# Optimization experiments

Measured on AMD Instinct MI355X. Metric: run time of the kernel, lower is better.

## Reference

```python
import jax, jax.numpy as jnp
import numpy as np

BATCH, L, IN_DIM, HID, STATE, MLP, OUT, NUM_LAYERS = 16, 2048, 64, 256, 256, 1024, 128, 4
MAX_PHASE = 2.0 * np.pi


def setup_inputs() -> dict:
    key = jax.random.key(0)
    ks = iter(jax.random.split(key, 32))
    x = jax.random.normal(next(ks), (BATCH, L, IN_DIM), dtype=jnp.float32)
    # embedding Linear(IN_DIM -> HID)
    emb_W = jax.random.normal(next(ks), (HID, IN_DIM), dtype=jnp.float32) / np.sqrt(IN_DIM)
    emb_b = jnp.zeros((HID,), dtype=jnp.float32)
    # LRU params per layer (r_min=0, r_max=1, max_phase=2pi)
    u1 = jax.random.uniform(next(ks), (NUM_LAYERS, STATE), minval=1e-4, maxval=1.0)
    u2 = jax.random.uniform(next(ks), (NUM_LAYERS, STATE), minval=1e-4, maxval=1.0)
    nu_log = jnp.log(-0.5 * jnp.log(u1))
    theta_log = jnp.log(MAX_PHASE * u2)
    lam_abs = jnp.exp(-jnp.exp(nu_log))
    gamma_log = jnp.log(jnp.sqrt(1.0 - lam_abs ** 2))
    B_re = jax.random.normal(next(ks), (NUM_LAYERS, STATE, HID)) / np.sqrt(2 * HID)
    B_im = jax.random.normal(next(ks), (NUM_LAYERS, STATE, HID)) / np.sqrt(2 * HID)
    C_re = jax.random.normal(next(ks), (NUM_LAYERS, HID, STATE)) / np.sqrt(STATE)
    C_im = jax.random.normal(next(ks), (NUM_LAYERS, HID, STATE)) / np.sqrt(STATE)
    D = jax.random.normal(next(ks), (NUM_LAYERS, HID))
    # block MLP: Linear(STATE->MLP), GELU, Linear(MLP->HID)
    Wh = jax.random.normal(next(ks), (NUM_LAYERS, MLP, STATE)) / np.sqrt(STATE)
    bh = jnp.zeros((NUM_LAYERS, MLP), dtype=jnp.float32)
    Wo = jax.random.normal(next(ks), (NUM_LAYERS, HID, MLP)) / np.sqrt(MLP)
    bo = jnp.zeros((NUM_LAYERS, HID), dtype=jnp.float32)
    # output Linear(HID -> OUT)
    out_W = jax.random.normal(next(ks), (OUT, HID), dtype=jnp.float32) / np.sqrt(HID)
    out_b = jnp.zeros((OUT,), dtype=jnp.float32)
    return {"x": x, "emb_W": emb_W, "emb_b": emb_b, "nu_log": nu_log,
            "theta_log": theta_log, "gamma_log": gamma_log, "B_re": B_re,
            "B_im": B_im, "C_re": C_re, "C_im": C_im, "D": D,
            "Wh": Wh, "bh": bh, "Wo": Wo, "bo": bo,
            "out_W": out_W, "out_b": out_b}


def _binop(ei, ej):
    a_i, bu_i = ei
    a_j, bu_j = ej
    return a_j * a_i, a_j * bu_i + bu_j


def _lru(x, nu, th, gl, Bre, Bim, Cre, Cim, D):
    # x: (B, L, H) real; state diag recurrence in complex64
    lam = jnp.exp(-jnp.exp(nu) + 1j * jnp.exp(th))               # (S,)
    B_norm = (Bre + 1j * Bim) * jnp.exp(gl)[:, None]             # (S, H)
    Bu = jnp.einsum("blh,sh->bls", x.astype(B_norm.dtype), B_norm)  # (B, L, S)
    Lam = jnp.broadcast_to(lam, Bu.shape)
    _, states = jax.lax.associative_scan(_binop, (Lam, Bu), axis=1)
    C = Cre + 1j * Cim                                           # (H, S)
    y = jnp.einsum("bls,hs->blh", states, C).real + D * x        # (B, L, H)
    return y


def reference(x, emb_W, emb_b, nu_log, theta_log, gamma_log, B_re, B_im,
              C_re, C_im, D, Wh, bh, Wo, bo, out_W, out_b):
    h = x @ emb_W.T + emb_b                                      # (B, L, HID)
    for l in range(NUM_LAYERS):
        y = _lru(h, nu_log[l], theta_log[l], gamma_log[l],
                 B_re[l], B_im[l], C_re[l], C_im[l], D[l])
        z = jax.nn.gelu(y @ Wh[l].T + bh[l], approximate=False)  # exact GELU as torch
        h = z @ Wo[l].T + bo[l] + y                              # residual
    return h @ out_W.T + out_b                                   # (B, L, OUT)
```

## Files before the change

kernel.cpp:

```cpp
#include <hip/hip_runtime.h>
#include <hip/hip_bf16.h>
#include <math.h>

typedef __hip_bfloat16 bf16;
typedef __attribute__((ext_vector_type(8))) short bf16x8;
typedef __attribute__((ext_vector_type(4))) float f32x4;

#define BATCH   16
#define SEQLEN  2048
#define INDIM   64
#define HIDD    256
#define STATE_D 256
#define MLPD    1024
#define OUTD    128
#define NLAYERS 4
#define M_TOK   (BATCH*SEQLEN)
#define CHUNK   64
#define NCHUNK  (SEQLEN/CHUNK)

__device__ float g_carry[512*512];
__device__ bf16  g_hb [(size_t)M_TOK*256];
__device__ bf16  g_yb [(size_t)M_TOK*256];
__device__ bf16  g_bub[(size_t)M_TOK*512];
__device__ bf16  g_zb [(size_t)M_TOK*1024];
__device__ bf16  g_Bnb[NLAYERS*512*256];
__device__ bf16  g_Cwb[NLAYERS*256*512];
__device__ bf16  g_Whb[NLAYERS*1024*256];
__device__ bf16  g_Wob[NLAYERS*256*1024];

#define SB_HB  0
#define SB_YB  1
#define SB_BUB 2
#define SB_ZB  3
#define SB_BNB 4
#define SB_CWB 5
#define SB_WHB 6
#define SB_WOB 7

__device__ __forceinline__ bf16* bufb(int sel){
  switch(sel){
    case SB_HB:  return g_hb;  case SB_YB:  return g_yb;
    case SB_BUB: return g_bub; case SB_ZB:  return g_zb;
    case SB_BNB: return g_Bnb; case SB_CWB: return g_Cwb;
    case SB_WHB: return g_Whb; default:     return g_Wob; }
}

__device__ __forceinline__ void gld_lds16(const void* g, void* l){
  __builtin_amdgcn_global_load_lds(
      (const __attribute__((address_space(1))) unsigned int*)g,
      (__attribute__((address_space(3))) unsigned int*)l, 16, 0, 0);
}

__device__ __forceinline__ float fast_gelu(float v){
  const float x  = v * 0.70710678118654752f;
  const float ax = fabsf(x);
  const float t  = __builtin_amdgcn_rcpf(fmaf(0.3275911f, ax, 1.0f));
  float p = fmaf(t, 1.061405429f, -1.453152027f);
  p = fmaf(t, p, 1.421413741f);
  p = fmaf(t, p, -0.284496736f);
  p = fmaf(t, p, 0.254829592f);
  p = p * t;
  const float e = __expf(-ax * ax);
  const float erf_ax = fmaf(-p, e, 1.0f);
  const float erf_x  = copysignf(erf_ax, x);
  return 0.5f * v * (1.0f + erf_x);
}

#define RPSTR 136

template<int ACT, int FLAGS>
__global__ __launch_bounds__(256, 6) void mfma_gemm(
    int aSel, int lda, int wSel, int wOff, int ldw,
    int oSel, int ldc,
    const float* __restrict__ bias,
    int rSel, int ldres,
    const float* __restrict__ dscale,
    int K)
{
  const bf16* A = bufb(aSel);
  const bf16* W = bufb(wSel) + wOff;
  bf16* OB = bufb(oSel);
  const bf16* res = (rSel >= 0) ? bufb(rSel) : nullptr;

  __shared__ __align__(16) unsigned short lds[12288];
  unsigned short* As = lds;
  unsigned short* Ws = lds + 4096;

  const int gx = gridDim.x;
  const int nwg = gx * gridDim.y;
  const int orig = blockIdx.y * gx + blockIdx.x;
  const int q = nwg >> 3, r = nwg & 7;
  const int xcd = orig & 7, idx = orig >> 3;
  const int wg = (xcd < r ? xcd*(q+1) : r*(q+1) + (xcd-r)*q) + idx;
  const int bx = wg % gx, by = wg / gx;

  const int tid  = threadIdx.x;
  const int row0 = by * 64, col0 = bx * 128;
  const int lane = tid & 63;
  const int m16  = lane & 15, quad = lane >> 4;
  const int wv   = tid >> 6;
  const int wm   = (wv & 1) * 32, wn = (wv >> 1) * 64;

  const int rlo = wv*16 + (lane >> 2);
  const int sg  = ((lane & 3) ^ ((rlo >> 1) & 3)) * 8;
  const bf16* ga = &A[(size_t)(row0 + rlo)*lda + sg];
  const bf16* gw = &W[(size_t)(col0 + rlo)*ldw + sg];
  const size_t w64 = (size_t)64 * ldw;

  auto STAGE = [&](int bb, int k0){
    unsigned short* Ab = As + bb*2048;
    unsigned short* Wb = Ws + bb*4096;
    gld_lds16(ga + k0,       Ab + wv*512);
    gld_lds16(gw + k0,       Wb + wv*512);
    gld_lds16(gw + k0 + w64, Wb + 2048 + wv*512);
  };

  f32x4 acc[2][4] = {};
  const int nt = K >> 5;

  STAGE(0, 0); STAGE(1, 32);

  for (int t = 0; t < nt; ++t){
    const int b = t & 1;
    if (t + 1 < nt) asm volatile("s_waitcnt vmcnt(3)" ::: "memory");
    else            asm volatile("s_waitcnt vmcnt(0)" ::: "memory");
    __builtin_amdgcn_s_barrier();

    const unsigned short* Ab = As + b*2048;
    const unsigned short* Wb = Ws + b*4096;
    bf16x8 af[2], wf[4];
    #pragma unroll
    for (int i = 0; i < 2; i++){
      const int rA = wm + 16*i + m16;
      af[i] = *reinterpret_cast<const bf16x8*>(&Ab[rA*32 + ((quad ^ ((rA>>1)&3))<<3)]);
    }
    #pragma unroll
    for (int j = 0; j < 4; j++){
      const int rW = wn + 16*j + m16;
      wf[j] = *reinterpret_cast<const bf16x8*>(&Wb[rW*32 + ((quad ^ ((rW>>1)&3))<<3)]);
    }
    asm volatile("s_waitcnt lgkmcnt(0)" ::: "memory");
    __builtin_amdgcn_sched_barrier(0);
    __builtin_amdgcn_s_barrier();

    if (t + 2 < nt) STAGE(b, (t + 2) << 5);

    __builtin_amdgcn_s_setprio(1);
    #pragma unroll
    for (int i = 0; i < 2; i++)
      #pragma unroll
      for (int j = 0; j < 4; j++)
        acc[i][j] = __builtin_amdgcn_mfma_f32_16x16x32_bf16(af[i], wf[j], acc[i][j], 0, 0, 0);
    __builtin_amdgcn_s_setprio(0);
  }

  #pragma unroll
  for (int i = 0; i < 2; i++){
    #pragma unroll
    for (int j = 0; j < 4; j++){
      const int lcol = wn + 16*j + m16;
      const int col  = col0 + lcol;
      #pragma unroll
      for (int r2 = 0; r2 < 4; r2++){
        const int lrow = wm + 16*i + quad*4 + r2;
        const int row  = row0 + lrow;
        float v = acc[i][j][r2];
        if (FLAGS & 1) v += bias[col];
        if (ACT == 1)  v = fast_gelu(v);
        if (FLAGS & 2) v += __bfloat162float(res[(size_t)row*ldres + col]);
        if (FLAGS & 4) v += dscale[col] * __bfloat162float(res[(size_t)row*ldres + col]);
        bf16 bv = __float2bfloat16(v);
        lds[lrow*RPSTR + lcol] = *reinterpret_cast<unsigned short*>(&bv);
      }
    }
  }
  __syncthreads();

  {
    const int rr  = tid >> 4;
    const int c16 = (tid & 15) * 8;
    #pragma unroll
    for (int s = 0; s < 4; s++){
      const int orow = s*16 + rr;
      uint4 d = *reinterpret_cast<const uint4*>(&lds[orow*RPSTR + c16]);
      *reinterpret_cast<uint4*>(OB + (size_t)(row0 + orow)*ldc + col0 + c16) = d;
    }
  }
}

__global__ __launch_bounds__(256) void emb_gemm(
    const float* __restrict__ x, const float* __restrict__ W,
    const float* __restrict__ b)
{
  __shared__ __align__(16) float Asx[16][68];
  __shared__ __align__(16) float Wsx[16][68];
  const int tid = threadIdx.x;
  const int tx = tid & 15, ty = tid >> 4;
  const int row0 = blockIdx.y * 64, col0 = blockIdx.x * 64;
  const int lc = tid & 15, lr = tid >> 4;
  float acc[4][4] = {};
  for (int k0 = 0; k0 < INDIM; k0 += 16){
    #pragma unroll
    for (int i = 0; i < 4; i++){
      Asx[lc][lr + 16*i] = x[(size_t)(row0 + lr + 16*i)*INDIM + k0 + lc];
      Wsx[lc][lr + 16*i] = W[(size_t)(col0 + lr + 16*i)*INDIM + k0 + lc];
    }
    __syncthreads();
    #pragma unroll
    for (int k = 0; k < 16; k++){
      float4 av = *reinterpret_cast<const float4*>(&Asx[k][ty*4]);
      float4 bv = *reinterpret_cast<const float4*>(&Wsx[k][tx*4]);
      float a[4] = {av.x, av.y, av.z, av.w};
      float b2[4] = {bv.x, bv.y, bv.z, bv.w};
      #pragma unroll
      for (int i = 0; i < 4; i++)
        #pragma unroll
        for (int j = 0; j < 4; j++)
          acc[i][j] = fmaf(a[i], b2[j], acc[i][j]);
    }
    __syncthreads();
  }
  #pragma unroll
  for (int i = 0; i < 4; i++){
    const int r = row0 + ty*4 + i;
    #pragma unroll
    for (int j = 0; j < 4; j++){
      const int cn = col0 + tx*4 + j;
      g_hb[(size_t)r*HIDD + cn] = __float2bfloat16(acc[i][j] + b[cn]);
    }
  }
}

__global__ __launch_bounds__(256) void out_gemm(
    const float* __restrict__ W, const float* __restrict__ b,
    float* __restrict__ out)
{
  __shared__ __align__(16) float Asx[16][68];
  __shared__ __align__(16) float Wsx[16][68];
  const int tid = threadIdx.x;
  const int tx = tid & 15, ty = tid >> 4;
  const int row0 = blockIdx.y * 64, col0 = blockIdx.x * 64;
  const int lc = tid & 15, lr = tid >> 4;
  float acc[4][4] = {};
  for (int k0 = 0; k0 < HIDD; k0 += 16){
    #pragma unroll
    for (int i = 0; i < 4; i++){
      Asx[lc][lr + 16*i] = __bfloat162float(g_hb[(size_t)(row0 + lr + 16*i)*HIDD + k0 + lc]);
      Wsx[lc][lr + 16*i] = W[(size_t)(col0 + lr + 16*i)*HIDD + k0 + lc];
    }
    __syncthreads();
    #pragma unroll
    for (int k = 0; k < 16; k++){
      float4 av = *reinterpret_cast<const float4*>(&Asx[k][ty*4]);
      float4 bv = *reinterpret_cast<const float4*>(&Wsx[k][tx*4]);
      float a[4] = {av.x, av.y, av.z, av.w};
      float b2[4] = {bv.x, bv.y, bv.z, bv.w};
      #pragma unroll
      for (int i = 0; i < 4; i++)
        #pragma unroll
        for (int j = 0; j < 4; j++)
          acc[i][j] = fmaf(a[i], b2[j], acc[i][j]);
    }
    __syncthreads();
  }
  #pragma unroll
  for (int i = 0; i < 4; i++){
    const int r = row0 + ty*4 + i;
    #pragma unroll
    for (int j = 0; j < 4; j++){
      const int cn = col0 + tx*4 + j;
      out[(size_t)r*OUTD + cn] = acc[i][j] + b[cn];
    }
  }
}

__device__ __forceinline__ void lam_of(const float* __restrict__ nu_log,
                                       const float* __restrict__ th_log,
                                       int s, float& lr, float& li)
{
  float nu  = expf(nu_log[s]);
  float th  = expf(th_log[s]);
  float mag = expf(-nu);
  lr = mag * cosf(th);
  li = mag * sinf(th);
}

__global__ __launch_bounds__(256) void scan_local(
    const float* __restrict__ nu_log, const float* __restrict__ th_log)
{
  const int blk = blockIdx.x;
  const int s   = threadIdx.x;
  float lr, li; lam_of(nu_log, th_log, s, lr, li);
  float ar = 0.f, ai = 0.f;
  size_t base = (size_t)blk * CHUNK * 512 + s;
  for (int t = 0; t < CHUNK; t++){
    float br = __bfloat162float(g_bub[base + (size_t)t*512]);
    float bi = __bfloat162float(g_bub[base + (size_t)t*512 + 256]);
    float nr = fmaf(lr, ar, fmaf(-li, ai, br));
    float ni = fmaf(lr, ai, fmaf( li, ar, bi));
    ar = nr; ai = ni;
  }
  g_carry[(size_t)blk*512 + s]       = ar;
  g_carry[(size_t)blk*512 + 256 + s] = ai;
}

__global__ __launch_bounds__(256) void scan_fix(
    const float* __restrict__ nu_log, const float* __restrict__ th_log)
{
  const int blk = blockIdx.x;
  const int c   = blk & (NCHUNK - 1);
  const int s   = threadIdx.x;
  float lr, li; lam_of(nu_log, th_log, s, lr, li);
  float cr = 0.f, ci = 0.f;
  if (c > 0){
    float Tr = lr, Ti = li;
    #pragma unroll
    for (int i = 0; i < 6; i++){ float nr = Tr*Tr - Ti*Ti; Ti = 2.f*Tr*Ti; Tr = nr; }
    const int bstart = blk - c;
    for (int j = 0; j < c; j++){
      float er = g_carry[(size_t)(bstart + j)*512 + s];
      float ei = g_carry[(size_t)(bstart + j)*512 + 256 + s];
      float nr = fmaf(Tr, cr, fmaf(-Ti, ci, er));
      float ni = fmaf(Tr, ci, fmaf( Ti, cr, ei));
      cr = nr; ci = ni;
    }
  }
  float ar = cr, ai = ci;
  size_t base = (size_t)blk * CHUNK * 512 + s;
  for (int t = 0; t < CHUNK; t++){
    size_t o = base + (size_t)t*512;
    float br = __bfloat162float(g_bub[o]);
    float bi = __bfloat162float(g_bub[o + 256]);
    float nr = fmaf(lr, ar, fmaf(-li, ai, br));
    float ni = fmaf(lr, ai, fmaf( li, ar, bi));
    ar = nr; ai = ni;
    g_bub[o]       = __float2bfloat16(ar);
    g_bub[o + 256] = __float2bfloat16(ai);
  }
}

__global__ __launch_bounds__(256) void pack_B(
    const float* __restrict__ Bre, const float* __restrict__ Bim,
    const float* __restrict__ gl)
{
  int idx = blockIdx.x * 256 + threadIdx.x;
  int l = idx >> 16, within = idx & 65535;
  int s = within >> 8;
  float g = expf(gl[l*STATE_D + s]);
  g_Bnb[(size_t)l*131072 + within]         = __float2bfloat16(Bre[idx] * g);
  g_Bnb[(size_t)l*131072 + 65536 + within] = __float2bfloat16(Bim[idx] * g);
}

__global__ __launch_bounds__(256) void pack_C(
    const float* __restrict__ Cre, const float* __restrict__ Cim)
{
  int idx = blockIdx.x * 256 + threadIdx.x;
  int l = idx >> 16, within = idx & 65535;
  int h = within >> 8, s = within & 255;
  g_Cwb[(size_t)l*131072 + (size_t)h*512 + s]       = __float2bfloat16( Cre[idx]);
  g_Cwb[(size_t)l*131072 + (size_t)h*512 + 256 + s] = __float2bfloat16(-Cim[idx]);
}

__global__ __launch_bounds__(256) void conv_bf16(
    const float* __restrict__ src, int dstSel, int n)
{
  int i = blockIdx.x * 256 + threadIdx.x;
  if (i < n) bufb(dstSel)[i] = __float2bfloat16(src[i]);
}

extern "C" void kernel_launch(void* const* d_in, const int* in_sizes, int n_in,
                              void* d_out, int out_size, void* d_ws, size_t ws_size,
                              hipStream_t stream)
{
  (void)d_ws; (void)ws_size; (void)out_size; (void)n_in; (void)in_sizes;
  const float* x      = (const float*)d_in[0];
  const float* emb_W  = (const float*)d_in[1];
  const float* emb_b  = (const float*)d_in[2];
  const float* nu_log = (const float*)d_in[3];
  const float* th_log = (const float*)d_in[4];
  const float* ga_log = (const float*)d_in[5];
  const float* B_re   = (const float*)d_in[6];
  const float* B_im   = (const float*)d_in[7];
  const float* C_re   = (const float*)d_in[8];
  const float* C_im   = (const float*)d_in[9];
  const float* Dv     = (const float*)d_in[10];
  const float* Wh     = (const float*)d_in[11];
  const float* bh     = (const float*)d_in[12];
  const float* Wo     = (const float*)d_in[13];
  const float* bo     = (const float*)d_in[14];
  const float* out_W  = (const float*)d_in[15];
  const float* out_b  = (const float*)d_in[16];

  const dim3 blk(256);

  pack_B<<<dim3(NLAYERS*256), blk, 0, stream>>>(B_re, B_im, ga_log);
  pack_C<<<dim3(NLAYERS*256), blk, 0, stream>>>(C_re, C_im);
  conv_bf16<<<dim3(NLAYERS*1024), blk, 0, stream>>>(Wh, SB_WHB, NLAYERS*262144);
  conv_bf16<<<dim3(NLAYERS*1024), blk, 0, stream>>>(Wo, SB_WOB, NLAYERS*262144);

  emb_gemm<<<dim3(HIDD/64, M_TOK/64), blk, 0, stream>>>(x, emb_W, emb_b);

  for (int l = 0; l < NLAYERS; l++){
    mfma_gemm<0, 0><<<dim3(4, M_TOK/64), blk, 0, stream>>>(
        SB_HB, HIDD, SB_BNB, l*131072, HIDD, SB_BUB, 512,
        nullptr, -1, 0, nullptr, HIDD);

    scan_local<<<dim3(M_TOK/CHUNK), blk, 0, stream>>>(nu_log + l*STATE_D, th_log + l*STATE_D);
    scan_fix  <<<dim3(M_TOK/CHUNK), blk, 0, stream>>>(nu_log + l*STATE_D, th_log + l*STATE_D);

    mfma_gemm<0, 4><<<dim3(2, M_TOK/64), blk, 0, stream>>>(
        SB_BUB, 512, SB_CWB, l*131072, 512, SB_YB, HIDD,
        nullptr, SB_HB, HIDD, Dv + l*HIDD, 512);

    mfma_gemm<1, 1><<<dim3(8, M_TOK/64), blk, 0, stream>>>(
        SB_YB, HIDD, SB_WHB, l*262144, STATE_D, SB_ZB, MLPD,
        bh + l*MLPD, -1, 0, nullptr, STATE_D);

    mfma_gemm<0, 3><<<dim3(2, M_TOK/64), blk, 0, stream>>>(
        SB_ZB, MLPD, SB_WOB, l*262144, MLPD, SB_HB, HIDD,
        bo + l*HIDD, SB_YB, HIDD, nullptr, MLPD);
  }

  out_gemm<<<dim3(OUTD/64, M_TOK/64), blk, 0, stream>>>(out_W, out_b, (float*)d_out);
}
```

Baseline: 836.9 us.

## Fuse chunk-local scan into Bu GEMM epilogue and interleave complex layout

The per-chunk carry computation (scan_local) now runs inside the Bu GEMM epilogue, reading the freshly computed 64-row tile from LDS instead of re-reading Bu from global memory in a separate kernel. B and C weights are repacked so real and imaginary parts are interleaved per state, which lets the scan kernels load and store each complex value as one 32-bit word. The cost is a serial 64-step loop on 64 threads at the end of each GEMM block, with the rest of the block idle during it.

```diff
diff --git a/kernel.cpp b/kernel.cpp
--- a/kernel.cpp
+++ b/kernel.cpp
@@ -66,6 +66,17 @@
   return 0.5f * v * (1.0f + erf_x);
 }
 
+__device__ __forceinline__ void lam_of(const float* __restrict__ nu_log,
+                                       const float* __restrict__ th_log,
+                                       int s, float& lr, float& li)
+{
+  float nu  = expf(nu_log[s]);
+  float th  = expf(th_log[s]);
+  float mag = expf(-nu);
+  lr = mag * cosf(th);
+  li = mag * sinf(th);
+}
+
 #define RPSTR 136
 
 template<int ACT, int FLAGS>
@@ -75,7 +86,9 @@
     const float* __restrict__ bias,
     int rSel, int ldres,
     const float* __restrict__ dscale,
-    int K)
+    int K,
+    const float* __restrict__ nu_log,
+    const float* __restrict__ th_log)
 {
   const bf16* A = bufb(aSel);
   const bf16* W = bufb(wSel) + wOff;
@@ -186,6 +199,24 @@
       *reinterpret_cast<uint4*>(OB + (size_t)(row0 + orow)*ldc + col0 + c16) = d;
     }
   }
+
+  if (FLAGS & 8){
+    if (tid < 64){
+      const int sglob = (col0 >> 1) + tid;
+      float lr, li; lam_of(nu_log, th_log, sglob, lr, li);
+      float ar = 0.f, ai = 0.f;
+      for (int t = 0; t < CHUNK; t++){
+        unsigned int pr = *reinterpret_cast<const unsigned int*>(&lds[t*RPSTR + 2*tid]);
+        float br = __uint_as_float(pr << 16);
+        float bi = __uint_as_float(pr & 0xffff0000u);
+        float nr = fmaf(lr, ar, fmaf(-li, ai, br));
+        float ni = fmaf(lr, ai, fmaf( li, ar, bi));
+        ar = nr; ai = ni;
+      }
+      g_carry[(size_t)by*512 + 2*sglob]     = ar;
+      g_carry[(size_t)by*512 + 2*sglob + 1] = ai;
+    }
+  }
 }
 
 __global__ __launch_bounds__(256) void emb_gemm(
@@ -274,36 +305,6 @@
   }
 }
 
-__device__ __forceinline__ void lam_of(const float* __restrict__ nu_log,
-                                       const float* __restrict__ th_log,
-                                       int s, float& lr, float& li)
-{
-  float nu  = expf(nu_log[s]);
-  float th  = expf(th_log[s]);
-  float mag = expf(-nu);
-  lr = mag * cosf(th);
-  li = mag * sinf(th);
-}
-
-__global__ __launch_bounds__(256) void scan_local(
-    const float* __restrict__ nu_log, const float* __restrict__ th_log)
-{
-  const int blk = blockIdx.x;
-  const int s   = threadIdx.x;
-  float lr, li; lam_of(nu_log, th_log, s, lr, li);
-  float ar = 0.f, ai = 0.f;
-  size_t base = (size_t)blk * CHUNK * 512 + s;
-  for (int t = 0; t < CHUNK; t++){
-    float br = __bfloat162float(g_bub[base + (size_t)t*512]);
-    float bi = __bfloat162float(g_bub[base + (size_t)t*512 + 256]);
-    float nr = fmaf(lr, ar, fmaf(-li, ai, br));
-    float ni = fmaf(lr, ai, fmaf( li, ar, bi));
-    ar = nr; ai = ni;
-  }
-  g_carry[(size_t)blk*512 + s]       = ar;
-  g_carry[(size_t)blk*512 + 256 + s] = ai;
-}
-
 __global__ __launch_bounds__(256) void scan_fix(
     const float* __restrict__ nu_log, const float* __restrict__ th_log)
 {
@@ -318,24 +319,25 @@
     for (int i = 0; i < 6; i++){ float nr = Tr*Tr - Ti*Ti; Ti = 2.f*Tr*Ti; Tr = nr; }
     const int bstart = blk - c;
     for (int j = 0; j < c; j++){
-      float er = g_carry[(size_t)(bstart + j)*512 + s];
-      float ei = g_carry[(size_t)(bstart + j)*512 + 256 + s];
-      float nr = fmaf(Tr, cr, fmaf(-Ti, ci, er));
-      float ni = fmaf(Tr, ci, fmaf( Ti, cr, ei));
+      float2 e = *reinterpret_cast<const float2*>(&g_carry[(size_t)(bstart + j)*512 + 2*s]);
+      float nr = fmaf(Tr, cr, fmaf(-Ti, ci, e.x));
+      float ni = fmaf(Tr, ci, fmaf( Ti, cr, e.y));
       cr = nr; ci = ni;
     }
   }
   float ar = cr, ai = ci;
-  size_t base = (size_t)blk * CHUNK * 512 + s;
+  unsigned int* pb = reinterpret_cast<unsigned int*>(g_bub) + (size_t)blk*CHUNK*256 + s;
   for (int t = 0; t < CHUNK; t++){
-    size_t o = base + (size_t)t*512;
-    float br = __bfloat162float(g_bub[o]);
-    float bi = __bfloat162float(g_bub[o + 256]);
+    unsigned int pr = pb[(size_t)t*256];
+    float br = __uint_as_float(pr << 16);
+    float bi = __uint_as_float(pr & 0xffff0000u);
     float nr = fmaf(lr, ar, fmaf(-li, ai, br));
     float ni = fmaf(lr, ai, fmaf( li, ar, bi));
     ar = nr; ai = ni;
-    g_bub[o]       = __float2bfloat16(ar);
-    g_bub[o + 256] = __float2bfloat16(ai);
+    bf16 hr = __float2bfloat16(ar), hi2 = __float2bfloat16(ai);
+    unsigned int w = (unsigned int)(*reinterpret_cast<unsigned short*>(&hr))
+                   | ((unsigned int)(*reinterpret_cast<unsigned short*>(&hi2)) << 16);
+    pb[(size_t)t*256] = w;
   }
 }
 
@@ -345,10 +347,10 @@
 {
   int idx = blockIdx.x * 256 + threadIdx.x;
   int l = idx >> 16, within = idx & 65535;
-  int s = within >> 8;
+  int s = within >> 8, h = within & 255;
   float g = expf(gl[l*STATE_D + s]);
-  g_Bnb[(size_t)l*131072 + within]         = __float2bfloat16(Bre[idx] * g);
-  g_Bnb[(size_t)l*131072 + 65536 + within] = __float2bfloat16(Bim[idx] * g);
+  g_Bnb[(size_t)l*131072 + (size_t)(2*s  )*256 + h] = __float2bfloat16(Bre[idx] * g);
+  g_Bnb[(size_t)l*131072 + (size_t)(2*s+1)*256 + h] = __float2bfloat16(Bim[idx] * g);
 }
 
 __global__ __launch_bounds__(256) void pack_C(
@@ -357,8 +359,8 @@
   int idx = blockIdx.x * 256 + threadIdx.x;
   int l = idx >> 16, within = idx & 65535;
   int h = within >> 8, s = within & 255;
-  g_Cwb[(size_t)l*131072 + (size_t)h*512 + s]       = __float2bfloat16( Cre[idx]);
-  g_Cwb[(size_t)l*131072 + (size_t)h*512 + 256 + s] = __float2bfloat16(-Cim[idx]);
+  g_Cwb[(size_t)l*131072 + (size_t)h*512 + 2*s]     = __float2bfloat16( Cre[idx]);
+  g_Cwb[(size_t)l*131072 + (size_t)h*512 + 2*s + 1] = __float2bfloat16(-Cim[idx]);
 }
 
 __global__ __launch_bounds__(256) void conv_bf16(
@@ -401,24 +403,24 @@
   emb_gemm<<<dim3(HIDD/64, M_TOK/64), blk, 0, stream>>>(x, emb_W, emb_b);
 
   for (int l = 0; l < NLAYERS; l++){
-    mfma_gemm<0, 0><<<dim3(4, M_TOK/64), blk, 0, stream>>>(
+    mfma_gemm<0, 8><<<dim3(4, M_TOK/64), blk, 0, stream>>>(
         SB_HB, HIDD, SB_BNB, l*131072, HIDD, SB_BUB, 512,
-        nullptr, -1, 0, nullptr, HIDD);
-
-    scan_local<<<dim3(M_TOK/CHUNK), blk, 0, stream>>>(nu_log + l*STATE_D, th_log + l*STATE_D);
-    scan_fix  <<<dim3(M_TOK/CHUNK), blk, 0, stream>>>(nu_log + l*STATE_D, th_log + l*STATE_D);
+        nullptr, -1, 0, nullptr, HIDD,
+        nu_log + l*STATE_D, th_log + l*STATE_D);
+
+    scan_fix<<<dim3(M_TOK/CHUNK), blk, 0, stream>>>(nu_log + l*STATE_D, th_log + l*STATE_D);
 
     mfma_gemm<0, 4><<<dim3(2, M_TOK/64), blk, 0, stream>>>(
         SB_BUB, 512, SB_CWB, l*131072, 512, SB_YB, HIDD,
-        nullptr, SB_HB, HIDD, Dv + l*HIDD, 512);
+        nullptr, SB_HB, HIDD, Dv + l*HIDD, 512, nullptr, nullptr);
 
     mfma_gemm<1, 1><<<dim3(8, M_TOK/64), blk, 0, stream>>>(
         SB_YB, HIDD, SB_WHB, l*262144, STATE_D, SB_ZB, MLPD,
-        bh + l*MLPD, -1, 0, nullptr, STATE_D);
+        bh + l*MLPD, -1, 0, nullptr, STATE_D, nullptr, nullptr);
 
     mfma_gemm<0, 3><<<dim3(2, M_TOK/64), blk, 0, stream>>>(
         SB_ZB, MLPD, SB_WOB, l*262144, MLPD, SB_HB, HIDD,
-        bo + l*HIDD, SB_YB, HIDD, nullptr, MLPD);
+        bo + l*HIDD, SB_YB, HIDD, nullptr, MLPD, nullptr, nullptr);
   }
 
   out_gemm<<<dim3(OUTD/64, M_TOK/64), blk, 0, stream>>>(out_W, out_b, (float*)d_out);
```

After: 809.9 us. 3.2% less time.
